# Performance work log

Measured on AMD Instinct MI355X. Metric: run time of the kernel, lower is better.

Reference implementation:

```python
import jax, jax.numpy as jnp
import numpy as np
import itertools

KH = KW = 3
N_NZ = 5
K_OUT = 126  # C(9,5) -> all patterns, matches capped n_kernels
C_IN = 128


def setup_inputs() -> dict:
    key = jax.random.key(0)
    k1, k2 = jax.random.split(key)
    inputs = jax.random.normal(k1, (32, 112, 112, C_IN), dtype=jnp.float32)
    # sparse_kernel: (n_non_zero, in_channels, kernels), glorot-ish scale
    scale = (2.0 / (N_NZ * C_IN + K_OUT)) ** 0.5
    sparse_kernel = jax.random.normal(k2, (N_NZ, C_IN, K_OUT), dtype=jnp.float32) * scale
    bias = jnp.zeros((K_OUT,), dtype=jnp.float32)
    # deterministic unique sparsity patterns: all C(9,5) flat-position combos
    patterns = jnp.asarray(
        np.array(list(itertools.combinations(range(KH * KW), N_NZ)), dtype=np.int32)
    )  # (K_OUT, N_NZ) flat positions in [0, 9)
    return {"inputs": inputs, "sparse_kernel": sparse_kernel, "bias": bias, "patterns": patterns}


def reference(inputs, sparse_kernel, bias, patterns):
    k_out = patterns.shape[0]
    c_in = sparse_kernel.shape[1]
    kk = jnp.arange(k_out)[:, None]  # (K,1) broadcasts against (K,N)
    # scatter: dense_flat[pos, :, k] = sparse_kernel[n, :, k]
    updates = jnp.transpose(sparse_kernel, (2, 0, 1))  # (K, N, Cin)
    dense_flat = jnp.zeros((KH * KW, c_in, k_out), dtype=inputs.dtype)
    dense_flat = dense_flat.at[patterns, :, kk].set(updates)
    dense_kernel = dense_flat.reshape(KH, KW, c_in, k_out)
    out = jax.lax.conv_general_dilated(
        inputs, dense_kernel, window_strides=(1, 1), padding="SAME",
        dimension_numbers=("NHWC", "HWIO", "NHWC"))
    return jax.nn.relu(out + bias)
```

## Files before the change

### kernel.cpp

```cpp
#include <hip/hip_runtime.h>


typedef __attribute__((ext_vector_type(8))) __bf16 bf16x8;
typedef __attribute__((ext_vector_type(4))) float f32x4;
typedef __attribute__((ext_vector_type(8))) unsigned short ushort8;

__device__ __forceinline__ unsigned short f2bf(float f) {
  unsigned int u = __builtin_bit_cast(unsigned int, f);
  u += 0x7fffu + ((u >> 16) & 1u);
  return (unsigned short)(u >> 16);
}

__device__ __forceinline__ void async_copy16(void* lds, const void* g) {
  __builtin_amdgcn_global_load_lds(
      (const __attribute__((address_space(1))) unsigned int*)g,
      (__attribute__((address_space(3))) unsigned int*)lds, 16, 0, 0);
}

#define BWS_BYTES 294912
#define ROW_BYTES 29184
#define ROW_USH   14592
#define AIN_BYTES (3584LL * ROW_BYTES)
#define WS_NEED   ((size_t)BWS_BYTES + (size_t)AIN_BYTES + (size_t)ROW_BYTES)

__global__ __launch_bounds__(256) void build_B(const float* __restrict__ sk,
                                               const int* __restrict__ patterns,
                                               unsigned short* __restrict__ Bws) {
  int idx = blockIdx.x * 256 + threadIdx.x;
  if (idx >= 9 * 128 * 128) return;
  int c = idx & 127;
  int n = (idx >> 7) & 127;
  int p = idx >> 14;
  float v = 0.f;
  if (n < 126) {
#pragma unroll
    for (int j = 0; j < 5; ++j)
      if (patterns[n * 5 + j] == p) v = sk[(j * 128 + c) * 126 + n];
  }
  int cc = c >> 5, cl = c & 31;
  Bws[(((p * 4 + cc) * 128) + n) * 32 + cl] = f2bf(v);
}

__global__ __launch_bounds__(256) void conv_pre(const float* __restrict__ in,
                                                unsigned short* __restrict__ Ain) {
  const int bid = ((blockIdx.x & 7) * 448) + (blockIdx.x >> 3);
  const float* inrow = in + (size_t)bid * 112 * 128;
  unsigned short* orow = Ain + (size_t)bid * ROW_USH;
  const int tid = threadIdx.x;
#pragma unroll
  for (int it = 0; it < 8; ++it) {
    int j = tid + it * 256;
    if (j < 1824) {
      int px = j >> 4;
      int ccq = j & 15;
      int gx = px - 1;
      ushort8 s = (ushort8)0;
      if ((unsigned)gx < 112u) {
        const float* p = inrow + (size_t)gx * 128 + ccq * 8;
        float4 a = *(const float4*)p;
        float4 b = *(const float4*)(p + 4);
        s[0] = f2bf(a.x); s[1] = f2bf(a.y); s[2] = f2bf(a.z); s[3] = f2bf(a.w);
        s[4] = f2bf(b.x); s[5] = f2bf(b.y); s[6] = f2bf(b.z); s[7] = f2bf(b.w);
      }
      int cc = ccq >> 2, q = ccq & 3;
      *(ushort8*)(orow + cc * 3648 + q * 912 + px * 8) = s;
    }
  }
}

__global__ __launch_bounds__(256, 3) void conv_main(const unsigned short* __restrict__ Ain,
                                                    const unsigned short* __restrict__ zp,
                                                    const unsigned short* __restrict__ Bws,
                                                    const float* __restrict__ bias,
                                                    float* __restrict__ out) {
  __shared__ unsigned short Alds[2 * 1536 * 8];

  const int tid = threadIdx.x;
  const int bid = ((blockIdx.x & 7) * 448) + (blockIdx.x >> 3);
  const int nimg = bid / 112;
  const int y = bid - nimg * 112;
  const int lane = tid & 63;
  const int w = tid >> 6;
  const int quad = lane >> 4;
  const int lrow = lane & 15;

  const unsigned short* rp0;
  const unsigned short* rp1 = Ain + (size_t)bid * ROW_USH;
  const unsigned short* rp2;
  rp0 = (y > 0)   ? (rp1 - ROW_USH) : zp;
  rp2 = (y < 111) ? (rp1 + ROW_USH) : zp;

  f32x4 acc[7][2];
#pragma unroll
  for (int mt = 0; mt < 7; ++mt) { acc[mt][0] = (f32x4)0.f; acc[mt][1] = (f32x4)0.f; }

  auto stage = [&](int cc, int buf) {
    const unsigned short* c0 = rp0 + cc * 3648;
    const unsigned short* c1 = rp1 + cc * 3648;
    const unsigned short* c2 = rp2 + cc * 3648;
#pragma unroll
    for (int it = 0; it < 6; ++it) {
      int i = tid + it * 256;
      bool b1 = (i >= 456), b2 = (i >= 912);
      int rem = i - (b2 ? 912 : (b1 ? 456 : 0));
      const unsigned short* base = b2 ? c2 : (b1 ? c1 : c0);
      const unsigned short* src = (i < 1368) ? (base + rem * 8) : zp;
      async_copy16((void*)&Alds[(size_t)buf * 12288 + (size_t)i * 8], (const void*)src);
    }
  };

  stage(0, 0);
  __syncthreads();

#pragma unroll 1
  for (int cc = 0; cc < 4; ++cc) {
    const int buf = cc & 1;
    bf16x8 b[9][2];
#pragma unroll
    for (int p = 0; p < 9; ++p)
#pragma unroll
      for (int j = 0; j < 2; ++j)
        b[p][j] = *(const bf16x8*)(Bws +
            (((size_t)(p * 4 + cc) * 128 + w * 32 + j * 16 + lrow) * 32 + quad * 8));

    if (cc < 3) stage(cc + 1, buf ^ 1);

#pragma unroll
    for (int p = 0; p < 9; ++p) {
      const int r = p / 3;
      const int px = p - r * 3;
      const int abase = buf * 12288 + r * 3648 + quad * 912 + (px + lrow) * 8;
#pragma unroll
      for (int mt = 0; mt < 7; ++mt) {
        bf16x8 a = *(const bf16x8*)&Alds[abase + mt * 128];
        acc[mt][0] = __builtin_amdgcn_mfma_f32_16x16x32_bf16(a, b[p][0], acc[mt][0], 0, 0, 0);
        acc[mt][1] = __builtin_amdgcn_mfma_f32_16x16x32_bf16(a, b[p][1], acc[mt][1], 0, 0, 0);
      }
    }

    if (cc < 3) __syncthreads();
  }

  const int k0 = w * 32 + lrow;
  const int k1 = k0 + 16;
  const float bv0 = bias[k0 < 126 ? k0 : 125];
  const float bv1 = bias[k1 < 126 ? k1 : 125];
  float* outrow = out + (size_t)bid * 112 * 126;
#pragma unroll
  for (int mt = 0; mt < 7; ++mt) {
#pragma unroll
    for (int rg = 0; rg < 4; ++rg) {
      int x = mt * 16 + quad * 4 + rg;
      float* o = outrow + (size_t)x * 126;
      if (k0 < 126) { float v = acc[mt][0][rg] + bv0; o[k0] = v > 0.f ? v : 0.f; }
      if (k1 < 126) { float v = acc[mt][1][rg] + bv1; o[k1] = v > 0.f ? v : 0.f; }
    }
  }
}

__global__ __launch_bounds__(256, 2) void conv_main_fb(const float* __restrict__ in,
                                                       const unsigned short* __restrict__ Bws,
                                                       const float* __restrict__ bias,
                                                       float* __restrict__ out) {
  __shared__ unsigned short Alds[2 * 4 * 342 * 8];

  const int tid = threadIdx.x;
  const int bid = ((blockIdx.x & 7) * 448) + (blockIdx.x >> 3);
  const int nimg = bid / 112;
  const int y = bid - nimg * 112;
  const int lane = tid & 63;
  const int w = tid >> 6;
  const int quad = lane >> 4;
  const int lrow = lane & 15;

  const float* inb = in + (size_t)nimg * 112 * 112 * 128;

  f32x4 acc[7][2];
#pragma unroll
  for (int mt = 0; mt < 7; ++mt) { acc[mt][0] = (f32x4)0.f; acc[mt][1] = (f32x4)0.f; }

  float4 pf[11];
  auto loadA = [&](int cc) {
#pragma unroll
    for (int it = 0; it < 11; ++it) {
      int i = tid + it * 256;
      float4 v = make_float4(0.f, 0.f, 0.f, 0.f);
      if (i < 2736) {
        int c4 = i & 7;
        int rest = i >> 3;
        int r = rest / 114;
        int hx = rest - r * 114;
        int gy = y + r - 1;
        int gx = hx - 1;
        if ((unsigned)gy < 112u && (unsigned)gx < 112u)
          v = *(const float4*)(inb + ((size_t)gy * 112 + gx) * 128 + cc * 32 + c4 * 4);
      }
      pf[it] = v;
    }
  };
  auto writeA = [&](int b) {
#pragma unroll
    for (int it = 0; it < 11; ++it) {
      int i = tid + it * 256;
      if (i < 2736) {
        int c4 = i & 7;
        int rest = i >> 3;
        int q = c4 >> 1, h = c4 & 1;
        ushort4 s;
        s.x = f2bf(pf[it].x); s.y = f2bf(pf[it].y);
        s.z = f2bf(pf[it].z); s.w = f2bf(pf[it].w);
        *(ushort4*)&Alds[(((b * 4 + q) * 342) + rest) * 8 + h * 4] = s;
      }
    }
  };

  loadA(0);
  writeA(0);
  __syncthreads();

#pragma unroll 1
  for (int cc = 0; cc < 4; ++cc) {
    const int cur = cc & 1;
    bf16x8 b[9][2];
#pragma unroll
    for (int p = 0; p < 9; ++p)
#pragma unroll
      for (int j = 0; j < 2; ++j)
        b[p][j] = *(const bf16x8*)(Bws +
            (((size_t)(p * 4 + cc) * 128 + w * 32 + j * 16 + lrow) * 32 + quad * 8));

    if (cc < 3) loadA(cc + 1);

    const unsigned short* Ab = &Alds[(size_t)(cur * 4 + quad) * 2736];
#pragma unroll
    for (int p = 0; p < 9; ++p) {
      const int r = p / 3;
      const int px = p - r * 3;
      const int abase = (r * 114 + px + lrow) * 8;
#pragma unroll
      for (int mt = 0; mt < 7; ++mt) {
        bf16x8 a = *(const bf16x8*)&Ab[abase + mt * 128];
        acc[mt][0] = __builtin_amdgcn_mfma_f32_16x16x32_bf16(a, b[p][0], acc[mt][0], 0, 0, 0);
        acc[mt][1] = __builtin_amdgcn_mfma_f32_16x16x32_bf16(a, b[p][1], acc[mt][1], 0, 0, 0);
      }
    }

    if (cc < 3) {
      writeA(cur ^ 1);
      __syncthreads();
    }
  }

  const int k0 = w * 32 + lrow;
  const int k1 = k0 + 16;
  const float bv0 = bias[k0 < 126 ? k0 : 125];
  const float bv1 = bias[k1 < 126 ? k1 : 125];
  float* outrow = out + (size_t)bid * 112 * 126;
#pragma unroll
  for (int mt = 0; mt < 7; ++mt) {
#pragma unroll
    for (int rg = 0; rg < 4; ++rg) {
      int x = mt * 16 + quad * 4 + rg;
      float* o = outrow + (size_t)x * 126;
      if (k0 < 126) { float v = acc[mt][0][rg] + bv0; o[k0] = v > 0.f ? v : 0.f; }
      if (k1 < 126) { float v = acc[mt][1][rg] + bv1; o[k1] = v > 0.f ? v : 0.f; }
    }
  }
}

extern "C" void kernel_launch(void* const* d_in, const int* in_sizes, int n_in,
                              void* d_out, int out_size, void* d_ws, size_t ws_size,
                              hipStream_t stream) {
  const float* in = (const float*)d_in[0];
  const float* sk = (const float*)d_in[1];
  const float* bias = (const float*)d_in[2];
  const int* patterns = (const int*)d_in[3];
  float* out = (float*)d_out;
  unsigned short* Bws = (unsigned short*)d_ws;

  build_B<<<dim3(576), dim3(256), 0, stream>>>(sk, patterns, Bws);

  if (ws_size >= WS_NEED) {
    unsigned short* Ain = (unsigned short*)((char*)d_ws + BWS_BYTES);
    unsigned short* zp  = (unsigned short*)((char*)d_ws + BWS_BYTES + AIN_BYTES);
    hipMemsetAsync(zp, 0, ROW_BYTES, stream);
    conv_pre<<<dim3(32 * 112), dim3(256), 0, stream>>>(in, Ain);
    conv_main<<<dim3(32 * 112), dim3(256), 0, stream>>>(Ain, zp, Bws, bias, out);
  } else {
    conv_main_fb<<<dim3(32 * 112), dim3(256), 0, stream>>>(in, Bws, bias, out);
  }
}
```

Before: 479.4 us.

## Retile conv_main to 2x2 wave grid and stage conv_pre through LDS

The main conv kernel moves from four waves each owning all 7 M-tiles and 32 output channels to a 2x2 wave grid: each wave covers up to 4 M-tiles and 64 channels. This raises reuse of each LDS A-fragment across more MFMAs, at the cost of more B registers (36 fragments) and occupancy lowered to 2 blocks per CU. The conversion kernel now reads input rows with coalesced float4 loads, packs them to bf16 with v_cvt_pk_bf16_f32 into an LDS transpose buffer, and then writes the output row contiguously. The output layout matches the previous cc/q/px ordering.

```diff
diff --git a/kernel.cpp b/kernel.cpp
--- a/kernel.cpp
+++ b/kernel.cpp
@@ -9,6 +9,12 @@
   unsigned int u = __builtin_bit_cast(unsigned int, f);
   u += 0x7fffu + ((u >> 16) & 1u);
   return (unsigned short)(u >> 16);
+}
+
+__device__ __forceinline__ unsigned int cvt_pk_bf16(float lo, float hi) {
+  unsigned int r;
+  asm("v_cvt_pk_bf16_f32 %0, %1, %2" : "=v"(r) : "v"(lo), "v"(hi));
+  return r;
 }
 
 __device__ __forceinline__ void async_copy16(void* lds, const void* g) {
@@ -43,32 +49,36 @@
 
 __global__ __launch_bounds__(256) void conv_pre(const float* __restrict__ in,
                                                 unsigned short* __restrict__ Ain) {
+  __shared__ unsigned short T[112 * 136];
   const int bid = ((blockIdx.x & 7) * 448) + (blockIdx.x >> 3);
   const float* inrow = in + (size_t)bid * 112 * 128;
   unsigned short* orow = Ain + (size_t)bid * ROW_USH;
   const int tid = threadIdx.x;
 #pragma unroll
+  for (int it = 0; it < 14; ++it) {
+    int i = tid + it * 256;
+    int px = i >> 5, c4 = i & 31;
+    float4 v = *(const float4*)(inrow + (size_t)i * 4);
+    unsigned int lo = cvt_pk_bf16(v.x, v.y);
+    unsigned int hi = cvt_pk_bf16(v.z, v.w);
+    *(uint2*)&T[px * 136 + c4 * 4] = make_uint2(lo, hi);
+  }
+  __syncthreads();
+#pragma unroll
   for (int it = 0; it < 8; ++it) {
-    int j = tid + it * 256;
-    if (j < 1824) {
-      int px = j >> 4;
-      int ccq = j & 15;
+    int o = tid + it * 256;
+    if (o < 1824) {
+      int ccq = o / 114;
+      int px = o - ccq * 114;
       int gx = px - 1;
       ushort8 s = (ushort8)0;
-      if ((unsigned)gx < 112u) {
-        const float* p = inrow + (size_t)gx * 128 + ccq * 8;
-        float4 a = *(const float4*)p;
-        float4 b = *(const float4*)(p + 4);
-        s[0] = f2bf(a.x); s[1] = f2bf(a.y); s[2] = f2bf(a.z); s[3] = f2bf(a.w);
-        s[4] = f2bf(b.x); s[5] = f2bf(b.y); s[6] = f2bf(b.z); s[7] = f2bf(b.w);
-      }
-      int cc = ccq >> 2, q = ccq & 3;
-      *(ushort8*)(orow + cc * 3648 + q * 912 + px * 8) = s;
-    }
-  }
-}
-
-__global__ __launch_bounds__(256, 3) void conv_main(const unsigned short* __restrict__ Ain,
+      if ((unsigned)gx < 112u) s = *(const ushort8*)&T[gx * 136 + ccq * 8];
+      *(ushort8*)(orow + (size_t)o * 8) = s;
+    }
+  }
+}
+
+__global__ __launch_bounds__(256, 2) void conv_main(const unsigned short* __restrict__ Ain,
                                                     const unsigned short* __restrict__ zp,
                                                     const unsigned short* __restrict__ Bws,
                                                     const float* __restrict__ bias,
@@ -77,22 +87,23 @@
 
   const int tid = threadIdx.x;
   const int bid = ((blockIdx.x & 7) * 448) + (blockIdx.x >> 3);
-  const int nimg = bid / 112;
-  const int y = bid - nimg * 112;
+  const int y = bid % 112;
   const int lane = tid & 63;
   const int w = tid >> 6;
+  const int wm = w >> 1;
+  const int wn = w & 1;
   const int quad = lane >> 4;
   const int lrow = lane & 15;
 
-  const unsigned short* rp0;
   const unsigned short* rp1 = Ain + (size_t)bid * ROW_USH;
-  const unsigned short* rp2;
-  rp0 = (y > 0)   ? (rp1 - ROW_USH) : zp;
-  rp2 = (y < 111) ? (rp1 + ROW_USH) : zp;
-
-  f32x4 acc[7][2];
-#pragma unroll
-  for (int mt = 0; mt < 7; ++mt) { acc[mt][0] = (f32x4)0.f; acc[mt][1] = (f32x4)0.f; }
+  const unsigned short* rp0 = (y > 0)   ? (rp1 - ROW_USH) : zp;
+  const unsigned short* rp2 = (y < 111) ? (rp1 + ROW_USH) : zp;
+
+  f32x4 acc[4][4];
+#pragma unroll
+  for (int mt = 0; mt < 4; ++mt)
+#pragma unroll
+    for (int j = 0; j < 4; ++j) acc[mt][j] = (f32x4)0.f;
 
   auto stage = [&](int cc, int buf) {
     const unsigned short* c0 = rp0 + cc * 3648;
@@ -115,45 +126,56 @@
 #pragma unroll 1
   for (int cc = 0; cc < 4; ++cc) {
     const int buf = cc & 1;
-    bf16x8 b[9][2];
+    bf16x8 b[9][4];
+    const unsigned short* Bb = Bws + (size_t)cc * 4096 + (wn * 64 + lrow) * 32 + quad * 8;
 #pragma unroll
     for (int p = 0; p < 9; ++p)
 #pragma unroll
-      for (int j = 0; j < 2; ++j)
-        b[p][j] = *(const bf16x8*)(Bws +
-            (((size_t)(p * 4 + cc) * 128 + w * 32 + j * 16 + lrow) * 32 + quad * 8));
+      for (int j = 0; j < 4; ++j)
+        b[p][j] = *(const bf16x8*)(Bb + p * 16384 + j * 512);
 
     if (cc < 3) stage(cc + 1, buf ^ 1);
 
 #pragma unroll
     for (int p = 0; p < 9; ++p) {
       const int r = p / 3;
-      const int px = p - r * 3;
-      const int abase = buf * 12288 + r * 3648 + quad * 912 + (px + lrow) * 8;
-#pragma unroll
-      for (int mt = 0; mt < 7; ++mt) {
-        bf16x8 a = *(const bf16x8*)&Alds[abase + mt * 128];
-        acc[mt][0] = __builtin_amdgcn_mfma_f32_16x16x32_bf16(a, b[p][0], acc[mt][0], 0, 0, 0);
-        acc[mt][1] = __builtin_amdgcn_mfma_f32_16x16x32_bf16(a, b[p][1], acc[mt][1], 0, 0, 0);
+      const int dx = p - r * 3;
+      const int abase = buf * 12288 + r * 3648 + quad * 912 + (dx + lrow) * 8 + wm * 512;
+#pragma unroll
+      for (int mt = 0; mt < 4; ++mt) {
+        if (mt < 3 || wm == 0) {
+          bf16x8 a = *(const bf16x8*)&Alds[abase + mt * 128];
+#pragma unroll
+          for (int j = 0; j < 4; ++j)
+            acc[mt][j] = __builtin_amdgcn_mfma_f32_16x16x32_bf16(a, b[p][j], acc[mt][j], 0, 0, 0);
+        }
       }
     }
 
     if (cc < 3) __syncthreads();
   }
 
-  const int k0 = w * 32 + lrow;
-  const int k1 = k0 + 16;
-  const float bv0 = bias[k0 < 126 ? k0 : 125];
-  const float bv1 = bias[k1 < 126 ? k1 : 125];
+  const int kb = wn * 64 + lrow;
+  float bv[4];
+#pragma unroll
+  for (int j = 0; j < 4; ++j) {
+    int k = kb + j * 16;
+    bv[j] = bias[k < 126 ? k : 125];
+  }
   float* outrow = out + (size_t)bid * 112 * 126;
 #pragma unroll
-  for (int mt = 0; mt < 7; ++mt) {
-#pragma unroll
-    for (int rg = 0; rg < 4; ++rg) {
-      int x = mt * 16 + quad * 4 + rg;
-      float* o = outrow + (size_t)x * 126;
-      if (k0 < 126) { float v = acc[mt][0][rg] + bv0; o[k0] = v > 0.f ? v : 0.f; }
-      if (k1 < 126) { float v = acc[mt][1][rg] + bv1; o[k1] = v > 0.f ? v : 0.f; }
+  for (int mt = 0; mt < 4; ++mt) {
+    if (mt < 3 || wm == 0) {
+#pragma unroll
+      for (int rg = 0; rg < 4; ++rg) {
+        int x = wm * 64 + mt * 16 + quad * 4 + rg;
+        float* o = outrow + (size_t)x * 126;
+#pragma unroll
+        for (int j = 0; j < 4; ++j) {
+          int k = kb + j * 16;
+          if (k < 126) { float v = acc[mt][j][rg] + bv[j]; o[k] = v > 0.f ? v : 0.f; }
+        }
+      }
     }
   }
 }
```

Result: slower. 507.6 us (+5.9%).
